# Kernel optimization log

Hardware: AMD Instinct MI355X
Metric: run time of the kernel (lower is better)

The kernel has to match this reference:

```python
import jax, jax.numpy as jnp
import numpy as np

NUM_EXPERTS = 8
TOP_K = 2
HIDDEN = 1024
FFN = 2048  # GLU width; h_to_4h projects to 2*FFN


def setup_inputs() -> dict:
    key = jax.random.key(0)
    k0, k1, k2, k3 = jax.random.split(key, 4)
    hidden_states = jax.random.normal(k0, (2048, 4, HIDDEN), dtype=jnp.float32)
    # router: nn.Linear(hidden, num_experts, bias=False) stored as [hidden, E]
    w_router = jax.random.normal(k1, (HIDDEN, NUM_EXPERTS), dtype=jnp.float32) * 0.02
    # per-expert dense_h_to_4h weights stacked: [E, hidden, 2*FFN]
    w1 = jax.random.normal(k2, (NUM_EXPERTS, HIDDEN, 2 * FFN), dtype=jnp.float32) * 0.02
    # per-expert dense_4h_to_h weights stacked: [E, FFN, hidden]
    w2 = jax.random.normal(k3, (NUM_EXPERTS, FFN, HIDDEN), dtype=jnp.float32) * 0.02
    return {"hidden_states": hidden_states, "w_router": w_router, "w1": w1, "w2": w2}


def reference(hidden_states, w_router, w1, w2):
    s, b, n = hidden_states.shape
    x = hidden_states.reshape(-1, n)              # [T, n], T = s*b
    T = x.shape[0]
    E = w1.shape[0]

    route = x @ w_router                          # [T, E] (router math in fp32)
    vals, idx = jax.lax.top_k(route, TOP_K)       # [T, k]
    gate_k = jax.nn.softmax(vals.astype(jnp.float32), axis=1).astype(x.dtype)
    # scatter top-k gates into dense [T, E] gate matrix (zeros elsewhere);
    # top_k indices are distinct per token so .set is exact
    gates = jnp.zeros((T, E), dtype=x.dtype).at[jnp.arange(T)[:, None], idx].set(gate_k)

    out = jnp.zeros_like(x)
    for e in range(E):  # small fixed expert count; each iter is one big GEMM pair
        h = x @ w1[e]                             # [T, 2*FFN]
        a, g = jnp.split(h, 2, axis=-1)
        act = a * jax.nn.silu(g)                  # swiglu
        out = out + gates[:, e:e + 1] * (act @ w2[e])
    return out.reshape(s, b, n)
```

## Files before the change

### kernel.cpp

```cpp
#include <hip/hip_runtime.h>
#include <hip/hip_bf16.h>
#include <math.h>


#define T_TOK 8192
#define HID   1024
#define NEXP  8
#define FFN   2048
#define PADU  256
#define MAXPAD (2 * T_TOK + NEXP * PADU)
#define MTG1   (MAXPAD / 256)
#define MTG2   (MAXPAD / 128)

typedef __attribute__((ext_vector_type(4))) float f32x4;
typedef __attribute__((ext_vector_type(8))) short bf16x8;
typedef __attribute__((ext_vector_type(8))) unsigned short u16x8;

static __device__ __forceinline__ unsigned short f2bf(float f) {
  unsigned int u = __float_as_uint(f);
  u += 0x7fffu + ((u >> 16) & 1u);
  return (unsigned short)(u >> 16);
}
static __device__ __forceinline__ float bf2f(unsigned short h) {
  return __uint_as_float(((unsigned int)h) << 16);
}

#define GLDS16(gsrc, ldst)                                                  \
  __builtin_amdgcn_global_load_lds(                                        \
      (const __attribute__((address_space(1))) void*)(gsrc),               \
      (__attribute__((address_space(3))) void*)(ldst), 16, 0, 0)

#define SFENCE() __builtin_amdgcn_sched_barrier(0)
#define BARRIER() do { SFENCE(); __builtin_amdgcn_s_barrier(); SFENCE(); } while (0)
#define LGKM0() do { asm volatile("s_waitcnt lgkmcnt(0)" ::: "memory"); SFENCE(); } while (0)
#define VMW(n) asm volatile("s_waitcnt vmcnt(" #n ")" ::: "memory")

__global__ __launch_bounds__(512) void k_router(
    const float* __restrict__ x, const float* __restrict__ wr,
    int* __restrict__ tok_idx, float* __restrict__ tok_gate) {
  __shared__ float wrT[8][1024];
  const int tid = threadIdx.x;
#pragma unroll
  for (int p = 0; p < 4; ++p) {
    const int idx = tid + p * 512;
    const float4 v = reinterpret_cast<const float4*>(wr)[idx];
    const int f = idx * 4;
    wrT[(f + 0) & 7][(f + 0) >> 3] = v.x;
    wrT[(f + 1) & 7][(f + 1) >> 3] = v.y;
    wrT[(f + 2) & 7][(f + 2) >> 3] = v.z;
    wrT[(f + 3) & 7][(f + 3) >> 3] = v.w;
  }
  __syncthreads();

  const int lane = tid & 63;
  const int wid  = tid >> 6;
  const int t    = blockIdx.x * 8 + wid;
  const float* xr = x + (size_t)t * HID;

  double acc[8] = {};
#pragma unroll
  for (int j = 0; j < 16; ++j) {
    const int k = lane + j * 64;
    const double xv = (double)xr[k];
#pragma unroll
    for (int e = 0; e < 8; ++e) acc[e] += xv * (double)wrT[e][k];
  }
#pragma unroll
  for (int e = 0; e < 8; ++e) {
#pragma unroll
    for (int off = 32; off > 0; off >>= 1) acc[e] += __shfl_down(acc[e], off);
  }
  if (lane == 0) {
    double v0 = -1e300, v1 = -1e300;
    int i0 = 0, i1 = 0;
#pragma unroll
    for (int e = 0; e < 8; ++e) {
      const double v = acc[e];
      if (v > v0)      { v1 = v0; i1 = i0; v0 = v; i0 = e; }
      else if (v > v1) { v1 = v; i1 = e; }
    }
    const float g0 = 1.0f / (1.0f + expf((float)(v1 - v0)));
    tok_idx[2 * t]     = i0;
    tok_idx[2 * t + 1] = i1;
    tok_gate[2 * t]     = g0;
    tok_gate[2 * t + 1] = 1.0f - g0;
  }
}

__global__ void k_count(const int* __restrict__ tok_idx, int* __restrict__ hdr) {
  __shared__ int h[8];
  const int tid = threadIdx.x;
  if (tid < 8) h[tid] = 0;
  __syncthreads();
  int c[8] = {0, 0, 0, 0, 0, 0, 0, 0};
  for (int i = tid; i < 2 * T_TOK; i += 256) {
    const int e = tok_idx[i];
#pragma unroll
    for (int q = 0; q < 8; ++q) c[q] += (e == q) ? 1 : 0;
  }
#pragma unroll
  for (int q = 0; q < 8; ++q) {
#pragma unroll
    for (int off = 32; off > 0; off >>= 1) c[q] += __shfl_down(c[q], off);
  }
  if ((tid & 63) == 0) {
#pragma unroll
    for (int q = 0; q < 8; ++q) atomicAdd(&h[q], c[q]);
  }
  __syncthreads();
  if (tid == 0) {
    int off = 0;
#pragma unroll
    for (int e = 0; e < 8; ++e) {
      hdr[e] = h[e];
      hdr[8 + e] = 0;
      hdr[16 + e] = off;
      off += (h[e] + PADU - 1) & ~(PADU - 1);
    }
    hdr[24] = off;
    hdr[25] = off;
  }
}

__global__ void k_scatter(const int* __restrict__ tok_idx, int* __restrict__ hdr,
                          int* __restrict__ bucket_tok, int* __restrict__ rowmap) {
  __shared__ int lcnt[8], lbase[8];
  const int tid = threadIdx.x;
  const int i = blockIdx.x * 256 + tid;
  const int e = tok_idx[i];
  if (tid < 8) lcnt[tid] = 0;
  __syncthreads();
  const int pos = atomicAdd(&lcnt[e], 1);
  __syncthreads();
  if (tid < 8) lbase[tid] = atomicAdd(&hdr[8 + tid], lcnt[tid]);
  __syncthreads();
  const int r = hdr[16 + e] + lbase[e] + pos;
  bucket_tok[r] = i >> 1;
  rowmap[i] = r;
}

__global__ void k_cvt_x(const float* __restrict__ x, unsigned short* __restrict__ xb) {
  const int i = blockIdx.x * 256 + threadIdx.x;
  const float4 v = reinterpret_cast<const float4*>(x)[i];
  ushort4 h;
  h.x = f2bf(v.x); h.y = f2bf(v.y); h.z = f2bf(v.z); h.w = f2bf(v.w);
  reinterpret_cast<ushort4*>(xb)[i] = h;
}

__global__ void k_cvtT(const float* __restrict__ src, unsigned short* __restrict__ dst,
                       int R, int C, int ilv) {
  const int e  = blockIdx.z;
  const int c0 = blockIdx.x * 64;
  const int r0 = blockIdx.y * 64;
  __shared__ unsigned short t[64][72];
  const int tid = threadIdx.x;
  const float* s = src + (size_t)e * R * C;
  unsigned short* d = dst + (size_t)e * R * C;
#pragma unroll
  for (int p = 0; p < 4; ++p) {
    const int idx = tid + p * 256;
    const int r  = idx >> 4;
    const int c4 = (idx & 15) << 2;
    const float4 v = *reinterpret_cast<const float4*>(s + (size_t)(r0 + r) * C + c0 + c4);
    t[c4 + 0][r] = f2bf(v.x); t[c4 + 1][r] = f2bf(v.y);
    t[c4 + 2][r] = f2bf(v.z); t[c4 + 3][r] = f2bf(v.w);
  }
  __syncthreads();
#pragma unroll
  for (int p = 0; p < 2; ++p) {
    const int idx = tid + p * 256;
    const int c  = idx >> 3;
    const int r8 = (idx & 7) << 3;
    u16x8 v;
#pragma unroll
    for (int i = 0; i < 8; ++i) v[i] = t[c][r8 + i];
    const int n = c0 + c;
    int row = n;
    if (ilv) {
      const int j = n & (FFN - 1);
      const int half = n >> 11;
      row = ((j >> 4) << 5) + (half << 4) + (j & 15);
    }
    *reinterpret_cast<u16x8*>(d + (size_t)row * R + r0 + r8) = v;
  }
}

__global__ __launch_bounds__(512, 2) void k_gemm1(
    const unsigned short* __restrict__ xb, const unsigned short* __restrict__ w1i,
    const int* __restrict__ bucket_tok, const int* __restrict__ hdr,
    unsigned short* __restrict__ act) {
  const int total = hdr[25];
  const int L    = blockIdx.y * 16 + blockIdx.x;
  const int xcd  = L & 7;
  const int slot = L >> 3;
  const int bx   = (xcd << 1) | (slot & 1);
  const int m0   = (slot >> 1) * 256;
  if (m0 >= total) return;
  int e = 0;
#pragma unroll
  for (int q = 1; q < 8; ++q) e += (m0 >= hdr[16 + q]) ? 1 : 0;
  const unsigned short* w1e = w1i + (size_t)e * 4096 * 1024;

  __shared__ __align__(16) char Lds[2 * 65536];

  const int tid  = threadIdx.x;
  const int lane = tid & 63;
  const int w    = tid >> 6;
  const int wm   = w >> 2;
  const int wn   = w & 3;
  const int lr   = lane & 15;
  const int qk16 = (lane >> 4) << 4;
  const int swz  = (lane & 7) << 4;
  const int kb0  = qk16 ^ swz;
  const int kb1  = (64 + qk16) ^ swz;

  const int r0 = w * 16 + (lane >> 3);
  const int cq = ((lane & 7) ^ (lane >> 3)) << 3;
  int aoff[2][2], boff[2][2];
#pragma unroll
  for (int h = 0; h < 2; ++h) {
    aoff[h][0] = bucket_tok[m0 + h * 128 + r0] * 1024 + cq;
    aoff[h][1] = bucket_tok[m0 + h * 128 + r0 + 8] * 1024 + cq;
    boff[h][0] = (bx * 256 + h * 128 + r0) * 1024 + cq;
    boff[h][1] = (bx * 256 + h * 128 + r0 + 8) * 1024 + cq;
  }
  const int ld0 = w * 2048 + lane * 16;

#define SA(dst, tt, h) do {                                                  \
    GLDS16(xb + aoff[h][0] + (tt) * 64, (dst) + (h) * 16384 + ld0);          \
    GLDS16(xb + aoff[h][1] + (tt) * 64, (dst) + (h) * 16384 + 1024 + ld0);   \
  } while (0)
#define SB(dst, tt, h) do {                                                  \
    GLDS16(w1e + boff[h][0] + (tt) * 64, (dst) + 32768 + (h) * 16384 + ld0); \
    GLDS16(w1e + boff[h][1] + (tt) * 64, (dst) + 32768 + (h) * 16384 + 1024 + ld0); \
  } while (0)

  f32x4 acc[8][4] = {};
  bf16x8 afq[4][2], bfr[4][2];

#define RD_A(M0) do {                                                        \
    _Pragma("unroll") for (int i = 0; i < 4; ++i) {                          \
      const int ra = wm * 128 + ((M0) + i) * 16 + lr;                        \
      afq[i][0] = *reinterpret_cast<const bf16x8*>(Ab + ra * 128 + kb0);     \
      afq[i][1] = *reinterpret_cast<const bf16x8*>(Ab + ra * 128 + kb1);     \
    } } while (0)
#define RD_B2(N0) do {                                                       \
    _Pragma("unroll") for (int i = 0; i < 2; ++i) {                          \
      const int rb = wn * 64 + ((N0) + i) * 16 + lr;                         \
      bfr[(N0) + i][0] = *reinterpret_cast<const bf16x8*>(Bb + rb * 128 + kb0); \
      bfr[(N0) + i][1] = *reinterpret_cast<const bf16x8*>(Bb + rb * 128 + kb1); \
    } } while (0)
#define QUAD(M0, N0) do {                                                    \
    __builtin_amdgcn_s_setprio(1);                                           \
    _Pragma("unroll") for (int mi = 0; mi < 4; ++mi)                         \
      _Pragma("unroll") for (int ni = 0; ni < 2; ++ni) {                     \
        acc[(M0) + mi][(N0) + ni] = __builtin_amdgcn_mfma_f32_16x16x32_bf16( \
            afq[mi][0], bfr[(N0) + ni][0], acc[(M0) + mi][(N0) + ni], 0, 0, 0); \
        acc[(M0) + mi][(N0) + ni] = __builtin_amdgcn_mfma_f32_16x16x32_bf16( \
            afq[mi][1], bfr[(N0) + ni][1], acc[(M0) + mi][(N0) + ni], 0, 0, 0); \
      }                                                                      \
    __builtin_amdgcn_s_setprio(0);                                           \
  } while (0)

  {
    char* D0 = Lds;
    char* D1 = Lds + 65536;
    SB(D0, 0, 0); SB(D0, 0, 1);
    SA(D0, 0, 0); SA(D0, 0, 1);
    SB(D1, 1, 0); SB(D1, 1, 1);
    SFENCE();
    VMW(4);
    BARRIER();
  }

  for (int t = 0; t < 16; ++t) {
    char* Ab = Lds + (t & 1) * 65536;
    char* Bb = Ab + 32768;
    char* Nb = Lds + ((t + 1) & 1) * 65536;
    RD_A(0); RD_B2(0);
    if (t < 15) SA(Nb, t + 1, 0);
    BARRIER(); LGKM0();
    QUAD(0, 0);
    BARRIER();
    RD_B2(2);
    if (t < 15) SA(Nb, t + 1, 1);
    BARRIER(); LGKM0();
    QUAD(0, 2);
    BARRIER();
    RD_A(4);
    if (t < 14) SB(Ab, t + 2, 0);
    BARRIER(); LGKM0();
    QUAD(4, 2);
    BARRIER();
    if (t < 14) SB(Ab, t + 2, 1);
    BARRIER();
    QUAD(4, 0);
    SFENCE();
    if (t < 14)      { VMW(4); }
    else if (t == 14) { VMW(0); }
    BARRIER();
  }
#undef SA
#undef SB
#undef RD_A
#undef RD_B2
#undef QUAD

  const int orow = (lane >> 4) << 2;
  const int baseCol = bx * 128 + wn * 32;
#pragma unroll
  for (int mi = 0; mi < 8; ++mi) {
#pragma unroll
    for (int p = 0; p < 2; ++p) {
      const f32x4 va = acc[mi][2 * p];
      const f32x4 vg = acc[mi][2 * p + 1];
#pragma unroll
      for (int r = 0; r < 4; ++r) {
        const float g = vg[r];
        const float v = va[r] * (g / (1.0f + expf(-g)));
        const int gm = m0 + wm * 128 + mi * 16 + orow + r;
        const int gc = baseCol + p * 16 + lr;
        act[(size_t)gm * FFN + gc] = f2bf(v);
      }
    }
  }
}

__global__ __launch_bounds__(512, 2) void k_gemm2(
    const unsigned short* __restrict__ act, const unsigned short* __restrict__ w2t,
    const int* __restrict__ hdr, unsigned short* __restrict__ y) {
  const int total = hdr[25];
  const int L  = blockIdx.y * 8 + blockIdx.x;
  const int m0 = (L >> 3) * 128;
  const int n0 = (L & 7) * 128;
  if (m0 >= total) return;
  int e = 0;
#pragma unroll
  for (int q = 1; q < 8; ++q) e += (m0 >= hdr[16 + q]) ? 1 : 0;
  const unsigned short* w2e = w2t + (size_t)e * 1024 * 2048;

  __shared__ __align__(16) char Lds[3 * 32768];

  const int tid  = threadIdx.x;
  const int lane = tid & 63;
  const int w    = tid >> 6;
  const int wrow = (w >> 2) * 64;
  const int wcol = (w & 3) * 32;
  const int lr   = lane & 15;
  const int qk16 = (lane >> 4) << 4;
  const int ldsw = w * 1024;

  const int srow = tid >> 3;
  const int cswz = (((tid & 7) ^ (srow & 7)) << 3);
  const int aoff0 = (m0 + srow) * FFN + cswz;
  const int boff0 = (n0 + srow) * FFN + cswz;

  f32x4 acc[4][2] = {};

#define G2_STAGE(base, kt) do {                                             \
    const unsigned short* as = act + (kt) * 64;                             \
    const unsigned short* ws = w2e + (kt) * 64;                             \
    GLDS16(as + aoff0,          Lds + (base) + ldsw);                       \
    GLDS16(as + aoff0 + 131072, Lds + (base) + 8192 + ldsw);                \
    GLDS16(ws + boff0,          Lds + (base) + 16384 + ldsw);               \
    GLDS16(ws + boff0 + 131072, Lds + (base) + 24576 + ldsw);               \
  } while (0)

  G2_STAGE(0, 0);
  G2_STAGE(32768, 1);
  SFENCE();
  asm volatile("s_waitcnt vmcnt(4)\n\ts_barrier" ::: "memory");
  SFENCE();

  int cur = 0, nxt2 = 2;
  for (int t = 0; t < 32; ++t) {
    const int pre = t + 2;
    if (pre < 32) {
      const int pb = ((cur + 2) >= 3 ? (cur - 1) : (cur + 2)) * 32768;
      G2_STAGE(pb, pre);
      SFENCE();
    }
    {
      const char* Ab = (const char*)Lds + cur * 32768;
      const char* Bb = Ab + 16384;
#pragma unroll
      for (int kk = 0; kk < 2; ++kk) {
        bf16x8 af[4], bv[2];
#pragma unroll
        for (int i = 0; i < 4; ++i) {
          const int ra = wrow + i * 16 + lr;
          af[i] = *reinterpret_cast<const bf16x8*>(Ab + ra * 128 + ((kk * 64 + qk16) ^ ((ra & 7) << 4)));
        }
#pragma unroll
        for (int i = 0; i < 2; ++i) {
          const int rb = wcol + i * 16 + lr;
          bv[i] = *reinterpret_cast<const bf16x8*>(Bb + rb * 128 + ((kk * 64 + qk16) ^ ((rb & 7) << 4)));
        }
        __builtin_amdgcn_s_setprio(1);
#pragma unroll
        for (int mi = 0; mi < 4; ++mi)
#pragma unroll
          for (int ni = 0; ni < 2; ++ni)
            acc[mi][ni] = __builtin_amdgcn_mfma_f32_16x16x32_bf16(af[mi], bv[ni], acc[mi][ni], 0, 0, 0);
        __builtin_amdgcn_s_setprio(0);
      }
    }
    SFENCE();
    if (pre < 32)      { asm volatile("s_waitcnt vmcnt(4)\n\ts_barrier" ::: "memory"); }
    else if (t + 1 < 32) { asm volatile("s_waitcnt vmcnt(0)\n\ts_barrier" ::: "memory"); }
    SFENCE();
    cur = (cur == 2) ? 0 : (cur + 1);
    nxt2 = (nxt2 == 2) ? 0 : (nxt2 + 1);
  }
#undef G2_STAGE

  const int orow = (lane >> 4) << 2;
#pragma unroll
  for (int mi = 0; mi < 4; ++mi)
#pragma unroll
    for (int ni = 0; ni < 2; ++ni)
#pragma unroll
      for (int r = 0; r < 4; ++r) {
        const int gm = m0 + wrow + mi * 16 + orow + r;
        const int gc = n0 + wcol + ni * 16 + lr;
        y[(size_t)gm * HID + gc] = f2bf(acc[mi][ni][r]);
      }
}

__global__ void k_combine(const unsigned short* __restrict__ y,
                          const int* __restrict__ rowmap,
                          const float* __restrict__ tok_gate,
                          float* __restrict__ out) {
  const int t = blockIdx.x;
  const int c = threadIdx.x << 2;
  const int r0 = rowmap[2 * t], r1 = rowmap[2 * t + 1];
  const float g0 = tok_gate[2 * t], g1 = tok_gate[2 * t + 1];
  const ushort4 a = *reinterpret_cast<const ushort4*>(y + (size_t)r0 * HID + c);
  const ushort4 b = *reinterpret_cast<const ushort4*>(y + (size_t)r1 * HID + c);
  float4 o;
  o.x = g0 * bf2f(a.x) + g1 * bf2f(b.x);
  o.y = g0 * bf2f(a.y) + g1 * bf2f(b.y);
  o.z = g0 * bf2f(a.z) + g1 * bf2f(b.z);
  o.w = g0 * bf2f(a.w) + g1 * bf2f(b.w);
  *reinterpret_cast<float4*>(out + (size_t)t * HID + c) = o;
}

extern "C" void kernel_launch(void* const* d_in, const int* in_sizes, int n_in,
                              void* d_out, int out_size, void* d_ws, size_t ws_size,
                              hipStream_t stream) {
  const float* x  = (const float*)d_in[0];
  const float* wr = (const float*)d_in[1];
  const float* w1 = (const float*)d_in[2];
  const float* w2 = (const float*)d_in[3];
  float* out = (float*)d_out;

  char* w = (char*)d_ws;
  int*   hdr        = (int*)w;
  int*   tok_idx    = (int*)(w + 1024);
  float* tok_gate   = (float*)(w + 1024 + 65536);
  int*   rowmap     = (int*)(w + 1024 + 2 * 65536);
  int*   bucket_tok = (int*)(w + 1024 + 3 * 65536);
  const size_t R1 = 524288;
  unsigned short* xb  = (unsigned short*)(w + R1);
  unsigned short* w1i = (unsigned short*)(w + R1 + 16777216);
  unsigned short* w2t = (unsigned short*)(w + R1);
  unsigned short* yb  = (unsigned short*)(w + R1 + 33554432);
  unsigned short* act = (unsigned short*)(w + R1 + 83886080);

  hipMemsetAsync(bucket_tok, 0, MAXPAD * sizeof(int), stream);

  k_router<<<T_TOK / 8, 512, 0, stream>>>(x, wr, tok_idx, tok_gate);
  k_count<<<1, 256, 0, stream>>>(tok_idx, hdr);
  k_scatter<<<(2 * T_TOK) / 256, 256, 0, stream>>>(tok_idx, hdr, bucket_tok, rowmap);
  k_cvt_x<<<(T_TOK * HID / 4) / 256, 256, 0, stream>>>(x, xb);
  k_cvtT<<<dim3(4096 / 64, 1024 / 64, 8), 256, 0, stream>>>(w1, w1i, 1024, 4096, 1);
  k_gemm1<<<dim3(16, MTG1), 512, 0, stream>>>(xb, w1i, bucket_tok, hdr, act);
  k_cvtT<<<dim3(1024 / 64, 2048 / 64, 8), 256, 0, stream>>>(w2, w2t, 2048, 1024, 0);
  k_gemm2<<<dim3(8, MTG2), 512, 0, stream>>>(act, w2t, hdr, yb);
  k_combine<<<T_TOK, 256, 0, stream>>>(yb, rowmap, tok_gate, out);
}
```

Measured before the change: 390.5 us.

## Fuse gated combine into second expert GEMM epilogue via atomic adds

Drops the separate combine kernel and the bf16 intermediate y buffer. The second GEMM epilogue now multiplies each row by a per-row gate, scattered earlier in k_scatter, and atomically adds the result into the zeroed fp32 output at the owning token. This removes a full write and read of y and one kernel launch, at the cost of an output memset and many fp32 atomics, with two contributors per output element. Padding rows are skipped through a zero gate.

```diff
diff --git a/kernel.cpp b/kernel.cpp
--- a/kernel.cpp
+++ b/kernel.cpp
@@ -122,8 +122,12 @@
   }
 }
 
-__global__ void k_scatter(const int* __restrict__ tok_idx, int* __restrict__ hdr,
-                          int* __restrict__ bucket_tok, int* __restrict__ rowmap) {
+__global__ void k_scatter(const int* __restrict__ tok_idx,
+                          const float* __restrict__ tok_gate,
+                          int* __restrict__ hdr,
+                          int* __restrict__ bucket_tok,
+                          float* __restrict__ row_gate,
+                          int* __restrict__ rowmap) {
   __shared__ int lcnt[8], lbase[8];
   const int tid = threadIdx.x;
   const int i = blockIdx.x * 256 + tid;
@@ -136,6 +140,7 @@
   __syncthreads();
   const int r = hdr[16 + e] + lbase[e] + pos;
   bucket_tok[r] = i >> 1;
+  row_gate[r] = tok_gate[i];
   rowmap[i] = r;
 }
 
@@ -328,7 +333,8 @@
 
 __global__ __launch_bounds__(512, 2) void k_gemm2(
     const unsigned short* __restrict__ act, const unsigned short* __restrict__ w2t,
-    const int* __restrict__ hdr, unsigned short* __restrict__ y) {
+    const int* __restrict__ hdr, const int* __restrict__ bucket_tok,
+    const float* __restrict__ row_gate, float* __restrict__ out) {
   const int total = hdr[25];
   const int L  = blockIdx.y * 8 + blockIdx.x;
   const int m0 = (L >> 3) * 128;
@@ -418,31 +424,19 @@
 #pragma unroll
   for (int mi = 0; mi < 4; ++mi)
 #pragma unroll
-    for (int ni = 0; ni < 2; ++ni)
-#pragma unroll
-      for (int r = 0; r < 4; ++r) {
-        const int gm = m0 + wrow + mi * 16 + orow + r;
-        const int gc = n0 + wcol + ni * 16 + lr;
-        y[(size_t)gm * HID + gc] = f2bf(acc[mi][ni][r]);
+    for (int r = 0; r < 4; ++r) {
+      const int gm = m0 + wrow + mi * 16 + orow + r;
+      const float g = row_gate[gm];
+      if (g != 0.0f) {
+        const int tok = bucket_tok[gm];
+        float* orow_p = out + (size_t)tok * HID;
+#pragma unroll
+        for (int ni = 0; ni < 2; ++ni) {
+          const int gc = n0 + wcol + ni * 16 + lr;
+          atomicAdd(orow_p + gc, g * acc[mi][ni][r]);
+        }
       }
-}
-
-__global__ void k_combine(const unsigned short* __restrict__ y,
-                          const int* __restrict__ rowmap,
-                          const float* __restrict__ tok_gate,
-                          float* __restrict__ out) {
-  const int t = blockIdx.x;
-  const int c = threadIdx.x << 2;
-  const int r0 = rowmap[2 * t], r1 = rowmap[2 * t + 1];
-  const float g0 = tok_gate[2 * t], g1 = tok_gate[2 * t + 1];
-  const ushort4 a = *reinterpret_cast<const ushort4*>(y + (size_t)r0 * HID + c);
-  const ushort4 b = *reinterpret_cast<const ushort4*>(y + (size_t)r1 * HID + c);
-  float4 o;
-  o.x = g0 * bf2f(a.x) + g1 * bf2f(b.x);
-  o.y = g0 * bf2f(a.y) + g1 * bf2f(b.y);
-  o.z = g0 * bf2f(a.z) + g1 * bf2f(b.z);
-  o.w = g0 * bf2f(a.w) + g1 * bf2f(b.w);
-  *reinterpret_cast<float4*>(out + (size_t)t * HID + c) = o;
+    }
 }
 
 extern "C" void kernel_launch(void* const* d_in, const int* in_sizes, int n_in,
@@ -460,22 +454,24 @@
   float* tok_gate   = (float*)(w + 1024 + 65536);
   int*   rowmap     = (int*)(w + 1024 + 2 * 65536);
   int*   bucket_tok = (int*)(w + 1024 + 3 * 65536);
+  float* row_gate   = (float*)(w + 1024 + 3 * 65536 + 73728);
   const size_t R1 = 524288;
   unsigned short* xb  = (unsigned short*)(w + R1);
   unsigned short* w1i = (unsigned short*)(w + R1 + 16777216);
   unsigned short* w2t = (unsigned short*)(w + R1);
-  unsigned short* yb  = (unsigned short*)(w + R1 + 33554432);
   unsigned short* act = (unsigned short*)(w + R1 + 83886080);
 
   hipMemsetAsync(bucket_tok, 0, MAXPAD * sizeof(int), stream);
+  hipMemsetAsync(row_gate, 0, MAXPAD * sizeof(float), stream);
+  hipMemsetAsync(out, 0, (size_t)T_TOK * HID * sizeof(float), stream);
 
   k_router<<<T_TOK / 8, 512, 0, stream>>>(x, wr, tok_idx, tok_gate);
   k_count<<<1, 256, 0, stream>>>(tok_idx, hdr);
-  k_scatter<<<(2 * T_TOK) / 256, 256, 0, stream>>>(tok_idx, hdr, bucket_tok, rowmap);
+  k_scatter<<<(2 * T_TOK) / 256, 256, 0, stream>>>(tok_idx, tok_gate, hdr,
+                                                   bucket_tok, row_gate, rowmap);
   k_cvt_x<<<(T_TOK * HID / 4) / 256, 256, 0, stream>>>(x, xb);
   k_cvtT<<<dim3(4096 / 64, 1024 / 64, 8), 256, 0, stream>>>(w1, w1i, 1024, 4096, 1);
   k_gemm1<<<dim3(16, MTG1), 512, 0, stream>>>(xb, w1i, bucket_tok, hdr, act);
   k_cvtT<<<dim3(1024 / 64, 2048 / 64, 8), 256, 0, stream>>>(w2, w2t, 2048, 1024, 0);
-  k_gemm2<<<dim3(8, MTG2), 512, 0, stream>>>(act, w2t, hdr, yb);
-  k_combine<<<T_TOK, 256, 0, stream>>>(yb, rowmap, tok_gate, out);
-}
+  k_gemm2<<<dim3(8, MTG2), 512, 0, stream>>>(act, w2t, hdr, bucket_tok, row_gate, out);
+}
```

Result: slower. 449.3 us (+15.1%).
